# Kernel tuning notes

Hardware: AMD Instinct MI355X
Metric: run time of the kernel (lower is better)

## Reference

```python
import jax, jax.numpy as jnp
import numpy as np
import math

D_MODEL = 2048
N_HEADS = 16
HEAD_DIM = D_MODEL // N_HEADS  # 128
SEQ = 2048
BATCH = 1


def make_freqs(seq_len, head_dim, theta=10000.0):
    # standard rotary frequencies: freqs_cis = exp(i * t * inv_freq)
    inv_freq = 1.0 / (theta ** (np.arange(0, head_dim, 2, dtype=np.float32) / head_dim))
    t = np.arange(seq_len, dtype=np.float32)
    ang = np.outer(t, inv_freq)  # [seq, head_dim/2]
    return jnp.asarray(np.cos(ang)), jnp.asarray(np.sin(ang))


def setup_inputs() -> dict:
    key = jax.random.key(0)
    ks = jax.random.split(key, 6)
    x = jax.random.normal(ks[0], (BATCH, SEQ, D_MODEL), dtype=jnp.float32)
    freqs_cos, freqs_sin = make_freqs(SEQ, HEAD_DIM)
    # causal additive mask, broadcastable to [b, h, s, s]
    mask = jnp.where(jnp.tril(jnp.ones((SEQ, SEQ), dtype=bool)), 0.0, -1e9).astype(jnp.float32)[None, None]
    scale = 0.02
    wq = jax.random.normal(ks[1], (D_MODEL, D_MODEL), dtype=jnp.float32) * scale
    wk = jax.random.normal(ks[2], (D_MODEL, D_MODEL), dtype=jnp.float32) * scale
    wv = jax.random.normal(ks[3], (D_MODEL, D_MODEL), dtype=jnp.float32) * scale
    wo = jax.random.normal(ks[4], (D_MODEL, D_MODEL), dtype=jnp.float32) * scale
    return {"x": x, "freqs_cos": freqs_cos, "freqs_sin": freqs_sin, "mask": mask,
            "wq": wq, "wk": wk, "wv": wv, "wo": wo}


def _apply_rotary(q, k, cos, sin):
    # q, k: [b, s, h, hd]; cos/sin: [s, hd/2]
    def rot(t):
        tr = t.reshape(*t.shape[:-1], -1, 2)  # [b, s, h, hd/2, 2]
        re, im = tr[..., 0], tr[..., 1]
        c = cos[None, :, None, :]
        s = sin[None, :, None, :]
        # complex multiply (re + i im) * (c + i s)
        out_re = re * c - im * s
        out_im = re * s + im * c
        return jnp.stack([out_re, out_im], axis=-1).reshape(t.shape)
    return rot(q), rot(k)


def reference(x, freqs_cos, freqs_sin, mask, wq, wk, wv, wo):
    b, s, _ = x.shape
    # QKV projections (nn.Linear with no bias: x @ W^T; W is square so use x @ W
    # with W stored already-transposed -- weights here are random so x @ W is faithful math)
    q = (x @ wq).reshape(b, s, N_HEADS, HEAD_DIM)
    k = (x @ wk).reshape(b, s, N_HEADS, HEAD_DIM)
    v = (x @ wv).reshape(b, s, N_HEADS, HEAD_DIM)
    q, k = _apply_rotary(q, k, freqs_cos, freqs_sin)
    # [b, h, s_q, s_k]
    scores = jnp.einsum("bqhd,bkhd->bhqk", q, k) / math.sqrt(HEAD_DIM)
    scores = scores + mask
    probs = jax.nn.softmax(scores.astype(jnp.float32), axis=-1).astype(q.dtype)
    out = jnp.einsum("bhqk,bkhd->bqhd", probs, v).reshape(b, s, N_HEADS * HEAD_DIM)
    return out @ wo
```

## Files before the change

kernel.cpp:

```cpp
#include <hip/hip_runtime.h>
#include <hip/hip_bf16.h>
#include <math.h>

#define SEQ 2048
#define DM 2048
#define NH 16
#define HD 128
#define QKV_N 6144

typedef __bf16 bf16;
typedef __bf16 bf16x8 __attribute__((ext_vector_type(8)));
typedef __bf16 bf16x4v __attribute__((ext_vector_type(4)));
typedef __bf16 bf16x2v __attribute__((ext_vector_type(2)));
typedef float f32x4 __attribute__((ext_vector_type(4)));

__device__ inline int sw_idx64(int row, int chunk) {
    return (row * 8 + (chunk ^ (row & 7))) * 8;
}
__device__ inline int sw_idx128(int row, int chunk) {
    return (row * 16 + (chunk ^ (row & 15))) * 8;
}

__device__ inline void async16(const void* g, void* l) {
    __builtin_amdgcn_global_load_lds((const __attribute__((address_space(1))) void*)g,
                                     (__attribute__((address_space(3))) void*)l, 16, 0, 0);
}

__global__ __launch_bounds__(256) void k_prep(const float* __restrict__ wq,
                                              const float* __restrict__ wk,
                                              const float* __restrict__ wv,
                                              const float* __restrict__ wo,
                                              bf16* __restrict__ wT, bf16* __restrict__ woT,
                                              const float* __restrict__ x,
                                              bf16* __restrict__ xb) {
    const int z = blockIdx.z;
    const int t = threadIdx.x;
    if (z == 4) {
        int bid = blockIdx.y * 32 + blockIdx.x;
#pragma unroll
        for (int j = 0; j < 4; ++j) {
            int i = bid * 1024 + j * 256 + t;
            float4 v = ((const float4*)x)[i];
            bf16x4v o;
            o.x = (bf16)v.x; o.y = (bf16)v.y; o.z = (bf16)v.z; o.w = (bf16)v.w;
            ((bf16x4v*)xb)[i] = o;
        }
        return;
    }
    __shared__ bf16 tile[64][66];
    const float* src = (z == 0) ? wq : (z == 1) ? wk : (z == 2) ? wv : wo;
    bf16* dst = (z < 3) ? (wT + (size_t)z * DM * DM) : woT;
    const int bx = blockIdx.x * 64, by = blockIdx.y * 64;
#pragma unroll
    for (int j = 0; j < 4; ++j) {
        int idx = j * 256 + t;
        int r = idx >> 4, cg = idx & 15;
        float4 v = *(const float4*)&src[(size_t)(by + r) * DM + bx + cg * 4];
        bf16x4v o;
        o.x = (bf16)v.x; o.y = (bf16)v.y; o.z = (bf16)v.z; o.w = (bf16)v.w;
        *(bf16x4v*)&tile[r][cg * 4] = o;
    }
    __syncthreads();
#pragma unroll
    for (int j = 0; j < 4; ++j) {
        int idx = j * 256 + t;
        int r = idx >> 4, cg = idx & 15;
        bf16x4v o;
        o.x = tile[cg * 4 + 0][r];
        o.y = tile[cg * 4 + 1][r];
        o.z = tile[cg * 4 + 2][r];
        o.w = tile[cg * 4 + 3][r];
        *(bf16x4v*)&dst[(size_t)(bx + r) * DM + by + cg * 4] = o;
    }
}

__global__ __launch_bounds__(256) void k_rope_vt(bf16* __restrict__ qkv,
                                                 const float* __restrict__ cosT,
                                                 const float* __restrict__ sinT,
                                                 bf16* __restrict__ vT) {
    const int t = threadIdx.x;
    if (blockIdx.x >= 1024) {
        int g = (blockIdx.x - 1024) * 256 + t;
        int s = g >> 8;
        int cg = g & 255;
        int h = cg >> 4, w8 = cg & 15;
        size_t base = (size_t)s * QKV_N + DM + h * HD + w8 * 8;
        float4 cv = *(const float4*)&cosT[s * 64 + w8 * 4];
        float4 sv = *(const float4*)&sinT[s * 64 + w8 * 4];
        float cc[4] = {cv.x, cv.y, cv.z, cv.w};
        float ss[4] = {sv.x, sv.y, sv.z, sv.w};
        bf16x8 k = *(bf16x8*)&qkv[base];
        bf16x8 o;
#pragma unroll
        for (int p = 0; p < 4; ++p) {
            float re = (float)k[2 * p], im = (float)k[2 * p + 1];
            o[2 * p]     = (bf16)(re * cc[p] - im * ss[p]);
            o[2 * p + 1] = (bf16)(re * ss[p] + im * cc[p]);
        }
        *(bf16x8*)&qkv[base] = o;
        return;
    }
    __shared__ bf16 tile[64][66];
    const int bx = (blockIdx.x & 31) * 64, by = (blockIdx.x >> 5) * 64;
#pragma unroll
    for (int j = 0; j < 4; ++j) {
        int idx = j * 256 + t;
        int r = idx >> 4, cg = idx & 15;
        *(bf16x4v*)&tile[r][cg * 4] =
            *(const bf16x4v*)&qkv[(size_t)(by + r) * QKV_N + 2 * DM + bx + cg * 4];
    }
    __syncthreads();
#pragma unroll
    for (int j = 0; j < 4; ++j) {
        int idx = j * 256 + t;
        int r = idx >> 4, cg = idx & 15;
        bf16x4v o;
        o.x = tile[cg * 4 + 0][r];
        o.y = tile[cg * 4 + 1][r];
        o.z = tile[cg * 4 + 2][r];
        o.w = tile[cg * 4 + 3][r];
        *(bf16x4v*)&vT[(size_t)(bx + r) * SEQ + by + cg * 4] = o;
    }
}

template <typename OutT, int BN>
__device__ __forceinline__ void gemm_body(const bf16* __restrict__ A,
                                          const bf16* __restrict__ Bt,
                                          OutT* __restrict__ C,
                                          int N, int K, size_t bm, size_t bn,
                                          bf16* As, bf16* Bs) {
    constexpr int NI = BN / 32;
    const int t = threadIdx.x;
    const int lane = t & 63;
    const int w = t >> 6;
    const int wr = (w >> 1) * 64, wc = (w & 1) * (BN / 2);
    const int l15 = lane & 15, quad = lane >> 4;
    f32x4 acc[4][NI];
#pragma unroll
    for (int i = 0; i < 4; ++i)
#pragma unroll
        for (int j = 0; j < NI; ++j) acc[i][j] = (f32x4){0.f, 0.f, 0.f, 0.f};

    for (int kt = 0; kt < K; kt += 64) {
#pragma unroll
        for (int j = 0; j < 4; ++j) {
            int c = j * 256 + t;
            int row = c >> 3, g = ((c & 7) ^ (row & 7)) * 8;
            async16(&A[(bm + row) * K + kt + g], &As[c * 8]);
        }
#pragma unroll
        for (int j = 0; j < NI; ++j) {
            int c = j * 256 + t;
            int row = c >> 3, g = ((c & 7) ^ (row & 7)) * 8;
            async16(&Bt[(bn + row) * K + kt + g], &Bs[c * 8]);
        }
        __syncthreads();
#pragma unroll
        for (int kh = 0; kh < 2; ++kh) {
            bf16x8 af[4], bfm[NI];
#pragma unroll
            for (int mi = 0; mi < 4; ++mi)
                af[mi] = *(const bf16x8*)&As[sw_idx64(wr + mi * 16 + l15, kh * 4 + quad)];
#pragma unroll
            for (int ni = 0; ni < NI; ++ni)
                bfm[ni] = *(const bf16x8*)&Bs[sw_idx64(wc + ni * 16 + l15, kh * 4 + quad)];
#pragma unroll
            for (int mi = 0; mi < 4; ++mi)
#pragma unroll
                for (int ni = 0; ni < NI; ++ni)
                    acc[mi][ni] = __builtin_amdgcn_mfma_f32_16x16x32_bf16(
                        af[mi], bfm[ni], acc[mi][ni], 0, 0, 0);
        }
        __syncthreads();
    }
#pragma unroll
    for (int mi = 0; mi < 4; ++mi)
#pragma unroll
        for (int ni = 0; ni < NI; ++ni)
#pragma unroll
            for (int r = 0; r < 4; ++r) {
                size_t row = bm + wr + mi * 16 + quad * 4 + r;
                size_t col = bn + wc + ni * 16 + l15;
                C[row * (size_t)N + col] = (OutT)acc[mi][ni][r];
            }
}

template <typename OutT, int BN>
__global__ __launch_bounds__(256) void k_gemm_bt(const bf16* __restrict__ A,
                                                 const bf16* __restrict__ Bt,
                                                 OutT* __restrict__ C,
                                                 int M, int N, int K) {
    __shared__ bf16 As[128 * 64];
    __shared__ bf16 Bs[BN * 64];
    size_t bm = (size_t)blockIdx.y * 128, bn = (size_t)blockIdx.x * BN;
    gemm_body<OutT, BN>(A, Bt, C, N, K, bm, bn, As, Bs);
}

__global__ __launch_bounds__(512) void k_flash(const bf16* __restrict__ qkv,
                                               const bf16* __restrict__ vT,
                                               const float* __restrict__ cosT,
                                               const float* __restrict__ sinT,
                                               bf16* __restrict__ out) {
    __shared__ bf16 Ks[2][64 * 128];
    __shared__ bf16 Vs[2][128 * 64];
    __shared__ bf16 Pl[8][16 * 64];
    const int t = threadIdx.x;
    const int lane = t & 63;
    const int w = t >> 6;
    const int wl = w & 3;
    const int g = w >> 2;
    const int l15 = lane & 15, quad = lane >> 4;
    const int b = blockIdx.x;
    const int hc = b & 15;
    const int h = (hc & 7) * 2 + (hc >> 3);
    const int p = b >> 4;
    const int qbH = 31 - p, qbL = p;
    const int myQb = g ? qbL : qbH;
    const int q0w = myQb * 64 + wl * 16;
    const float sc2 = 0.08838834764831845f * 1.4426950408889634f;

    const size_t qrow = (size_t)(q0w + l15) * QKV_N + h * HD;
    bf16x8 aq[4];
#pragma unroll
    for (int u = 0; u < 4; ++u)
        aq[u] = *(const bf16x8*)&qkv[qrow + u * 32 + quad * 8];
#pragma unroll
    for (int u = 0; u < 4; ++u) {
        float4 cv = *(const float4*)&cosT[(q0w + l15) * 64 + u * 16 + quad * 4];
        float4 sv = *(const float4*)&sinT[(q0w + l15) * 64 + u * 16 + quad * 4];
        float cc[4] = {cv.x, cv.y, cv.z, cv.w};
        float ss[4] = {sv.x, sv.y, sv.z, sv.w};
        bf16x8 q = aq[u], rq;
#pragma unroll
        for (int pp = 0; pp < 4; ++pp) {
            float re = (float)q[2 * pp], im = (float)q[2 * pp + 1];
            rq[2 * pp]     = (bf16)(re * cc[pp] - im * ss[pp]);
            rq[2 * pp + 1] = (bf16)(re * ss[pp] + im * cc[pp]);
        }
        aq[u] = rq;
    }

    f32x4 o[8];
#pragma unroll
    for (int c = 0; c < 8; ++c) o[c] = (f32x4){0.f, 0.f, 0.f, 0.f};
    float l_r[4] = {0.f, 0.f, 0.f, 0.f};

    int krow[2], kg[2], vrow[2], vg[2];
#pragma unroll
    for (int j = 0; j < 2; ++j) {
        int c2 = j * 512 + t;
        krow[j] = c2 >> 4; kg[j] = ((c2 & 15) ^ (krow[j] & 15)) * 8;
        vrow[j] = c2 >> 3; vg[j] = ((c2 & 7) ^ (vrow[j] & 7)) * 8;
    }
    auto stage = [&](int buf, int kt2) {
        const int kb2 = kt2 * 64;
#pragma unroll
        for (int j = 0; j < 2; ++j)
            async16(&qkv[(size_t)(kb2 + krow[j]) * QKV_N + DM + h * HD + kg[j]],
                    &Ks[buf][(j * 512 + t) * 8]);
#pragma unroll
        for (int j = 0; j < 2; ++j)
            async16(&vT[(size_t)(h * HD + vrow[j]) * SEQ + kb2 + vg[j]],
                    &Vs[buf][(j * 512 + t) * 8]);
    };

    const int nT = qbH + 1;
    stage(0, 0);
    for (int kt = 0; kt < nT; ++kt) {
        const int cb = kt & 1;
        const int kbase = kt * 64;
        const bool pre = (kt + 1 < nT);
        if (pre) {
            stage(cb ^ 1, kt + 1);
            asm volatile("s_waitcnt vmcnt(6)" ::: "memory");
        } else {
            asm volatile("s_waitcnt vmcnt(2)" ::: "memory");
        }
        __builtin_amdgcn_s_barrier();
        asm volatile("" ::: "memory");

        const bool active = (kt <= myQb);
        if (active) {
            f32x4 s4[4];
            __builtin_amdgcn_s_setprio(1);
#pragma unroll
            for (int sub = 0; sub < 4; ++sub) {
                f32x4 z = (f32x4){0.f, 0.f, 0.f, 0.f};
#pragma unroll
                for (int u = 0; u < 4; ++u) {
                    bf16x8 kv = *(const bf16x8*)&Ks[cb][sw_idx128(sub * 16 + l15, u * 4 + quad)];
                    z = __builtin_amdgcn_mfma_f32_16x16x32_bf16(aq[u], kv, z, 0, 0, 0);
                }
                s4[sub] = z;
            }
            __builtin_amdgcn_s_setprio(0);
            const bool masked = (kt == myQb);
#pragma unroll
            for (int sub = 0; sub < 4; ++sub)
#pragma unroll
                for (int r = 0; r < 4; ++r) {
                    float pv = __builtin_amdgcn_exp2f(s4[sub][r] * sc2);
                    if (masked)
                        pv = (kbase + sub * 16 + l15 <= q0w + quad * 4 + r) ? pv : 0.f;
                    l_r[r] += pv;
                    int rowp = quad * 4 + r;
                    int col = sub * 16 + l15;
                    Pl[w][(rowp * 8 + ((col >> 3) ^ (rowp & 7))) * 8 + (col & 7)] = (bf16)pv;
                }
        }
        if (pre) asm volatile("s_waitcnt vmcnt(4)" ::: "memory");
        else     asm volatile("s_waitcnt vmcnt(0)" ::: "memory");
        __builtin_amdgcn_s_barrier();
        if (active) {
            __asm__ __volatile__("s_waitcnt lgkmcnt(0)" ::: "memory");
            bf16x8 pf[2];
#pragma unroll
            for (int kk = 0; kk < 2; ++kk)
                pf[kk] = *(const bf16x8*)&Pl[w][sw_idx64(l15, kk * 4 + quad)];
            __builtin_amdgcn_s_setprio(1);
#pragma unroll
            for (int c = 0; c < 8; ++c)
#pragma unroll
                for (int kk = 0; kk < 2; ++kk) {
                    bf16x8 vb = *(const bf16x8*)&Vs[cb][sw_idx64(c * 16 + l15, kk * 4 + quad)];
                    o[c] = __builtin_amdgcn_mfma_f32_16x16x32_bf16(pf[kk], vb, o[c], 0, 0, 0);
                }
            __builtin_amdgcn_s_setprio(0);
        }
        asm volatile("" ::: "memory");
        __builtin_amdgcn_s_barrier();
        asm volatile("" ::: "memory");
    }

    float rl[4];
#pragma unroll
    for (int r = 0; r < 4; ++r) {
        float l = l_r[r];
        l += __shfl_xor(l, 1, 16);
        l += __shfl_xor(l, 2, 16);
        l += __shfl_xor(l, 4, 16);
        l += __shfl_xor(l, 8, 16);
        rl[r] = 1.0f / l;
    }
#pragma unroll
    for (int c = 0; c < 8; ++c)
#pragma unroll
        for (int r = 0; r < 4; ++r)
            out[(size_t)(q0w + quad * 4 + r) * DM + h * HD + c * 16 + l15] =
                (bf16)(o[c][r] * rl[r]);
}

extern "C" void kernel_launch(void* const* d_in, const int* in_sizes, int n_in,
                              void* d_out, int out_size, void* d_ws, size_t ws_size,
                              hipStream_t stream) {
    const float* x  = (const float*)d_in[0];
    const float* fc = (const float*)d_in[1];
    const float* fs = (const float*)d_in[2];
    const float* wq = (const float*)d_in[4];
    const float* wk = (const float*)d_in[5];
    const float* wv = (const float*)d_in[6];
    const float* wo = (const float*)d_in[7];
    float* out = (float*)d_out;

    char* ws = (char*)d_ws;
    bf16* xb  = (bf16*)(ws);
    bf16* wT  = (bf16*)(ws + (size_t)(8u  << 20));
    bf16* woT = (bf16*)(ws + (size_t)(32u << 20));
    bf16* qkv = (bf16*)(ws + (size_t)(40u << 20));
    bf16* vT  = (bf16*)(ws + (size_t)(64u << 20));

    k_prep<<<dim3(32, 32, 5), 256, 0, stream>>>(wq, wk, wv, wo, wT, woT, x, xb);
    k_gemm_bt<bf16, 128><<<dim3(48, 16), 256, 0, stream>>>(xb, wT, qkv, SEQ, QKV_N, DM);
    k_rope_vt<<<3072, 256, 0, stream>>>(qkv, fc, fs, vT);
    k_flash<<<256, 512, 0, stream>>>(qkv, vT, fc, fs, xb);
    k_gemm_bt<float, 64><<<dim3(32, 16), 256, 0, stream>>>(xb, woT, out, SEQ, DM, DM);
}
```

Measured before the change: 290.8 us.

## Split flash attention KV tiles across wave groups and double block count

Previously each 512-thread block paired a heavy and a light query block across its two wave groups. Now each block handles a single query block, and the two wave groups split each 64-key tile into two 32-key halves. The partial outputs and row sums are combined through shared memory at the end, and the grid doubles to 512 blocks. The aim is to remove idle waves in the lighter group and raise parallelism, at the cost of an LDS reduction epilogue and less MFMA work per barrier.

```diff
diff --git a/kernel.cpp b/kernel.cpp
--- a/kernel.cpp
+++ b/kernel.cpp
@@ -19,6 +19,9 @@
 }
 __device__ inline int sw_idx128(int row, int chunk) {
     return (row * 16 + (chunk ^ (row & 15))) * 8;
+}
+__device__ inline int sw_idx32(int row, int chunk) {
+    return (row * 4 + (chunk ^ (row & 3))) * 8;
 }
 
 __device__ inline void async16(const void* g, void* l) {
@@ -203,7 +206,7 @@
                                                bf16* __restrict__ out) {
     __shared__ bf16 Ks[2][64 * 128];
     __shared__ bf16 Vs[2][128 * 64];
-    __shared__ bf16 Pl[8][16 * 64];
+    __shared__ bf16 Pl[8][16 * 32];
     const int t = threadIdx.x;
     const int lane = t & 63;
     const int w = t >> 6;
@@ -213,10 +216,8 @@
     const int b = blockIdx.x;
     const int hc = b & 15;
     const int h = (hc & 7) * 2 + (hc >> 3);
-    const int p = b >> 4;
-    const int qbH = 31 - p, qbL = p;
-    const int myQb = g ? qbL : qbH;
-    const int q0w = myQb * 64 + wl * 16;
+    const int qb = (b < 256) ? (31 - (b >> 4)) : ((b >> 4) - 16);
+    const int q0w = qb * 64 + wl * 16;
     const float sc2 = 0.08838834764831845f * 1.4426950408889634f;
 
     const size_t qrow = (size_t)(q0w + l15) * QKV_N + h * HD;
@@ -264,7 +265,7 @@
                     &Vs[buf][(j * 512 + t) * 8]);
     };
 
-    const int nT = qbH + 1;
+    const int nT = qb + 1;
     stage(0, 0);
     for (int kt = 0; kt < nT; ++kt) {
         const int cb = kt & 1;
@@ -279,75 +280,89 @@
         __builtin_amdgcn_s_barrier();
         asm volatile("" ::: "memory");
 
-        const bool active = (kt <= myQb);
-        if (active) {
-            f32x4 s4[4];
-            __builtin_amdgcn_s_setprio(1);
-#pragma unroll
-            for (int sub = 0; sub < 4; ++sub) {
-                f32x4 z = (f32x4){0.f, 0.f, 0.f, 0.f};
-#pragma unroll
-                for (int u = 0; u < 4; ++u) {
-                    bf16x8 kv = *(const bf16x8*)&Ks[cb][sw_idx128(sub * 16 + l15, u * 4 + quad)];
-                    z = __builtin_amdgcn_mfma_f32_16x16x32_bf16(aq[u], kv, z, 0, 0, 0);
-                }
-                s4[sub] = z;
+        f32x4 s4[2];
+        __builtin_amdgcn_s_setprio(1);
+#pragma unroll
+        for (int sl = 0; sl < 2; ++sl) {
+            const int sub = 2 * g + sl;
+            f32x4 z = (f32x4){0.f, 0.f, 0.f, 0.f};
+#pragma unroll
+            for (int u = 0; u < 4; ++u) {
+                bf16x8 kv = *(const bf16x8*)&Ks[cb][sw_idx128(sub * 16 + l15, u * 4 + quad)];
+                z = __builtin_amdgcn_mfma_f32_16x16x32_bf16(aq[u], kv, z, 0, 0, 0);
             }
-            __builtin_amdgcn_s_setprio(0);
-            const bool masked = (kt == myQb);
-#pragma unroll
-            for (int sub = 0; sub < 4; ++sub)
-#pragma unroll
-                for (int r = 0; r < 4; ++r) {
-                    float pv = __builtin_amdgcn_exp2f(s4[sub][r] * sc2);
-                    if (masked)
-                        pv = (kbase + sub * 16 + l15 <= q0w + quad * 4 + r) ? pv : 0.f;
-                    l_r[r] += pv;
-                    int rowp = quad * 4 + r;
-                    int col = sub * 16 + l15;
-                    Pl[w][(rowp * 8 + ((col >> 3) ^ (rowp & 7))) * 8 + (col & 7)] = (bf16)pv;
-                }
+            s4[sl] = z;
+        }
+        __builtin_amdgcn_s_setprio(0);
+        const bool masked = (kt == qb);
+#pragma unroll
+        for (int sl = 0; sl < 2; ++sl) {
+            const int sub = 2 * g + sl;
+#pragma unroll
+            for (int r = 0; r < 4; ++r) {
+                float pv = __builtin_amdgcn_exp2f(s4[sl][r] * sc2);
+                if (masked)
+                    pv = (kbase + sub * 16 + l15 <= q0w + quad * 4 + r) ? pv : 0.f;
+                l_r[r] += pv;
+                int rowp = quad * 4 + r;
+                int lc = sl * 16 + l15;
+                Pl[w][(rowp * 4 + ((lc >> 3) ^ (rowp & 3))) * 8 + (lc & 7)] = (bf16)pv;
+            }
         }
         if (pre) asm volatile("s_waitcnt vmcnt(4)" ::: "memory");
         else     asm volatile("s_waitcnt vmcnt(0)" ::: "memory");
         __builtin_amdgcn_s_barrier();
-        if (active) {
-            __asm__ __volatile__("s_waitcnt lgkmcnt(0)" ::: "memory");
-            bf16x8 pf[2];
-#pragma unroll
-            for (int kk = 0; kk < 2; ++kk)
-                pf[kk] = *(const bf16x8*)&Pl[w][sw_idx64(l15, kk * 4 + quad)];
-            __builtin_amdgcn_s_setprio(1);
-#pragma unroll
-            for (int c = 0; c < 8; ++c)
-#pragma unroll
-                for (int kk = 0; kk < 2; ++kk) {
-                    bf16x8 vb = *(const bf16x8*)&Vs[cb][sw_idx64(c * 16 + l15, kk * 4 + quad)];
-                    o[c] = __builtin_amdgcn_mfma_f32_16x16x32_bf16(pf[kk], vb, o[c], 0, 0, 0);
-                }
-            __builtin_amdgcn_s_setprio(0);
-        }
+        __asm__ __volatile__("s_waitcnt lgkmcnt(0)" ::: "memory");
+        bf16x8 pf = *(const bf16x8*)&Pl[w][sw_idx32(l15, quad)];
+        __builtin_amdgcn_s_setprio(1);
+#pragma unroll
+        for (int c = 0; c < 8; ++c) {
+            bf16x8 vb = *(const bf16x8*)&Vs[cb][sw_idx64(c * 16 + l15, g * 4 + quad)];
+            o[c] = __builtin_amdgcn_mfma_f32_16x16x32_bf16(pf, vb, o[c], 0, 0, 0);
+        }
+        __builtin_amdgcn_s_setprio(0);
         asm volatile("" ::: "memory");
         __builtin_amdgcn_s_barrier();
         asm volatile("" ::: "memory");
     }
 
-    float rl[4];
-#pragma unroll
-    for (int r = 0; r < 4; ++r) {
-        float l = l_r[r];
-        l += __shfl_xor(l, 1, 16);
-        l += __shfl_xor(l, 2, 16);
-        l += __shfl_xor(l, 4, 16);
-        l += __shfl_xor(l, 8, 16);
-        rl[r] = 1.0f / l;
-    }
-#pragma unroll
-    for (int c = 0; c < 8; ++c)
-#pragma unroll
-        for (int r = 0; r < 4; ++r)
-            out[(size_t)(q0w + quad * 4 + r) * DM + h * HD + c * 16 + l15] =
-                (bf16)(o[c][r] * rl[r]);
+    __syncthreads();
+    float* oxch = (float*)&Ks[0][0];
+    float* lxch = (float*)&Pl[0][0];
+    const int tp = t & 255;
+    if (g == 1) {
+#pragma unroll
+        for (int c = 0; c < 8; ++c)
+            *(f32x4*)&oxch[tp * 32 + c * 4] = o[c];
+#pragma unroll
+        for (int r = 0; r < 4; ++r) lxch[tp * 4 + r] = l_r[r];
+    }
+    __syncthreads();
+    if (g == 0) {
+#pragma unroll
+        for (int c = 0; c < 8; ++c) {
+            f32x4 v = *(const f32x4*)&oxch[tp * 32 + c * 4];
+            o[c] += v;
+        }
+#pragma unroll
+        for (int r = 0; r < 4; ++r) l_r[r] += lxch[tp * 4 + r];
+        float rl[4];
+#pragma unroll
+        for (int r = 0; r < 4; ++r) {
+            float l = l_r[r];
+            l += __shfl_xor(l, 1, 16);
+            l += __shfl_xor(l, 2, 16);
+            l += __shfl_xor(l, 4, 16);
+            l += __shfl_xor(l, 8, 16);
+            rl[r] = 1.0f / l;
+        }
+#pragma unroll
+        for (int c = 0; c < 8; ++c)
+#pragma unroll
+            for (int r = 0; r < 4; ++r)
+                out[(size_t)(q0w + quad * 4 + r) * DM + h * HD + c * 16 + l15] =
+                    (bf16)(o[c][r] * rl[r]);
+    }
 }
 
 extern "C" void kernel_launch(void* const* d_in, const int* in_sizes, int n_in,
@@ -372,6 +387,6 @@
     k_prep<<<dim3(32, 32, 5), 256, 0, stream>>>(wq, wk, wv, wo, wT, woT, x, xb);
     k_gemm_bt<bf16, 128><<<dim3(48, 16), 256, 0, stream>>>(xb, wT, qkv, SEQ, QKV_N, DM);
     k_rope_vt<<<3072, 256, 0, stream>>>(qkv, fc, fs, vT);
-    k_flash<<<256, 512, 0, stream>>>(qkv, vT, fc, fs, xb);
+    k_flash<<<512, 512, 0, stream>>>(qkv, vT, fc, fs, xb);
     k_gemm_bt<float, 64><<<dim3(32, 16), 256, 0, stream>>>(xb, woT, out, SEQ, DM, DM);
 }
```

Measured after the change: 282.9 us. 1.03x faster.
